# Kernel optimization log

Hardware: AMD Instinct MI355X
Metric: run time of the kernel (lower is better)

The kernel has to match this reference:

```python
import jax, jax.numpy as jnp
import numpy as np

N, K, D = 131072, 1024, 128
COMMITMENT_COST = 0.25


def setup_inputs() -> dict:
    key = jax.random.key(0)
    k1, k2 = jax.random.split(key)
    c_input = jax.random.normal(k1, (N, D), dtype=jnp.float32)
    # nn.Embedding weight initialized N(0, 0.1)
    embedding_weight = jax.random.normal(k2, (K, D), dtype=jnp.float32) * 0.1
    return {"c_input": c_input, "embedding_weight": embedding_weight}


def reference(c_input, embedding_weight):
    distances = (
        jnp.sum(c_input ** 2, axis=1, keepdims=True)
        + jnp.sum(embedding_weight ** 2, axis=1)
        - 2.0 * jnp.matmul(c_input, embedding_weight.T)
    )
    encoding_indices = jnp.argmin(distances, axis=1)  # [N]
    encodings = jax.nn.one_hot(encoding_indices, K, dtype=c_input.dtype)  # [N, K]
    # one-hot @ weight == direct gather
    quantized = embedding_weight[encoding_indices]  # [N, D]
    e_latent_loss = jnp.mean((jax.lax.stop_gradient(quantized) - c_input) ** 2)
    q_latent_loss = jnp.mean((quantized - jax.lax.stop_gradient(c_input)) ** 2)
    loss = q_latent_loss + COMMITMENT_COST * e_latent_loss
    # straight-through estimator
    quantized_st = c_input + jax.lax.stop_gradient(quantized - c_input)
    return (loss, quantized_st, encodings)
```

## Files before the change

kernel.cpp:

```cpp
#include <hip/hip_runtime.h>
#include <hip/hip_bf16.h>

#define NROWS 131072
#define KC 1024
#define DD 128
#define MARGIN 1e-3f

typedef __attribute__((ext_vector_type(8))) short short8;
typedef __attribute__((ext_vector_type(4))) float f32x4;

__device__ inline short f2bf_hi(float f) {
  unsigned u = __builtin_bit_cast(unsigned, f);
  u += 0x7fffu + ((u >> 16) & 1u);
  return (short)(u >> 16);
}
__device__ inline float bf2f(short s) {
  unsigned u = ((unsigned)(unsigned short)s) << 16;
  return __builtin_bit_cast(float, u);
}

__global__ void vq_prep(const float* __restrict__ E, short* __restrict__ EH,
                        short* __restrict__ EL, float* __restrict__ SE,
                        float* __restrict__ out) {
  int b = blockIdx.x, t = threadIdx.x;
  if (b < 64) {
    int idx = b * 256 + t;
    int s = (idx >> 6) & 3, l = idx & 63;
    int c = idx >> 8;
    int q = l >> 4, n = l & 15;
    const float* src = E + (16 * c + n) * DD + 32 * s + 8 * q;
    short8 h, lo;
#pragma unroll
    for (int j = 0; j < 8; ++j) {
      float x = src[j];
      short hb = f2bf_hi(x);
      h[j] = hb;
      lo[j] = f2bf_hi(x - bf2f(hb));
    }
    *(short8*)(EH + idx * 8) = h;
    *(short8*)(EL + idx * 8) = lo;
  } else {
    if (t == 0) out[0] = 0.f;
    for (int k = t; k < KC; k += 256) {
      double acc = 0.0;
      const float* er = E + k * DD;
      for (int i = 0; i < DD; ++i) { double v = (double)er[i]; acc += v * v; }
      SE[k] = (float)acc;
    }
  }
}

__global__ __launch_bounds__(256, 4) void vq_main(
    const float* __restrict__ X, const float* __restrict__ E,
    const short* __restrict__ EH, const short* __restrict__ EL,
    const float* __restrict__ SE, float* __restrict__ out) {
  __shared__ __align__(16) short lbh[8192];
  __shared__ __align__(16) short lbl[8192];
  __shared__ __align__(16) float lse[KC];
  __shared__ int lidx[128];
  __shared__ int lflag[128];
  __shared__ int lany;
  __shared__ float lx[128];
  __shared__ float lrv[4];
  __shared__ int lri[4];
  __shared__ float lsx;
  __shared__ float lloss[4];

  const int tid = threadIdx.x;
  const int w = tid >> 6, l = tid & 63, q = l >> 4, n = l & 15;
  const int row_base = blockIdx.x * 128;
  const int rot = blockIdx.x & 15;
  const int encb = 1 + NROWS * DD;
  if (tid == 0) lany = 0;
  *(f32x4*)(lse + tid * 4) = *(const f32x4*)(SE + tid * 4);

  float* zb = out + encb + row_base * KC;
  if (tid < 3) __builtin_nontemporal_store(0.f, zb + tid);
  else if (tid == 3) __builtin_nontemporal_store(0.f, zb + 131071);
  float* zb4 = zb + 3;

  short8 ah[2][4], al[2][4];
#pragma unroll
  for (int mt = 0; mt < 2; ++mt) {
    const float* xp = X + (row_base + 32 * w + 16 * mt + n) * DD + 8 * q;
#pragma unroll
    for (int s = 0; s < 4; ++s) {
      f32x4 x0 = *(const f32x4*)(xp + 32 * s);
      f32x4 x1 = *(const f32x4*)(xp + 32 * s + 4);
#pragma unroll
      for (int j = 0; j < 4; ++j) {
        short hb = f2bf_hi(x0[j]);
        ah[mt][s][j] = hb;
        al[mt][s][j] = f2bf_hi(x0[j] - bf2f(hb));
        short hb2 = f2bf_hi(x1[j]);
        ah[mt][s][j + 4] = hb2;
        al[mt][s][j + 4] = f2bf_hi(x1[j] - bf2f(hb2));
      }
    }
  }

  float bestv[8], secv[8];
  int besti[8];
#pragma unroll
  for (int i = 0; i < 8; ++i) { bestv[i] = -3e38f; secv[i] = -3e38f; besti[i] = 0; }

  const f32x4 z4 = {0.f, 0.f, 0.f, 0.f};
  for (int cc = 0; cc < 16; ++cc) {
    const int ccr = (cc + rot) & 15;
    {
      const short8* gh = (const short8*)(EH + ccr * 8192);
      const short8* gl = (const short8*)(EL + ccr * 8192);
      short8* dh = (short8*)lbh;
      short8* dl = (short8*)lbl;
#pragma unroll
      for (int i = 0; i < 4; ++i) {
        int u = i * 256 + tid;
        dh[u] = gh[u];
        dl[u] = gl[u];
      }
    }
    __syncthreads();

    {
      int jb = cc * 2048 + tid;
#pragma unroll
      for (int u2 = 0; u2 < 8; ++u2) {
        int j = jb + u2 * 256;
        if (j < 32767) __builtin_nontemporal_store(z4, (f32x4*)(zb4 + 4 * j));
      }
    }

#pragma unroll
    for (int nt = 0; nt < 4; ++nt) {
      f32x4 a0 = {0.f, 0.f, 0.f, 0.f}, a1 = {0.f, 0.f, 0.f, 0.f};
#pragma unroll
      for (int s = 0; s < 4; ++s) {
        short8 bh  = *(const short8*)(lbh + ((nt * 4 + s) * 64 + l) * 8);
        short8 blo = *(const short8*)(lbl + ((nt * 4 + s) * 64 + l) * 8);
        a0 = __builtin_amdgcn_mfma_f32_16x16x32_bf16(ah[0][s], bh,  a0, 0, 0, 0);
        a1 = __builtin_amdgcn_mfma_f32_16x16x32_bf16(ah[1][s], bh,  a1, 0, 0, 0);
        a0 = __builtin_amdgcn_mfma_f32_16x16x32_bf16(al[0][s], bh,  a0, 0, 0, 0);
        a1 = __builtin_amdgcn_mfma_f32_16x16x32_bf16(al[1][s], bh,  a1, 0, 0, 0);
        a0 = __builtin_amdgcn_mfma_f32_16x16x32_bf16(ah[0][s], blo, a0, 0, 0, 0);
        a1 = __builtin_amdgcn_mfma_f32_16x16x32_bf16(ah[1][s], blo, a1, 0, 0, 0);
      }
      int k = ccr * 64 + nt * 16 + n;
      float hse = 0.5f * lse[k];
#pragma unroll
      for (int r = 0; r < 4; ++r) {
        {
          float sc = a0[r] - hse;
          bool gt = sc > bestv[r];
          secv[r] = gt ? bestv[r] : fmaxf(secv[r], sc);
          if (gt) { bestv[r] = sc; besti[r] = k; }
        }
        {
          int sl = 4 + r;
          float sc = a1[r] - hse;
          bool gt = sc > bestv[sl];
          secv[sl] = gt ? bestv[sl] : fmaxf(secv[sl], sc);
          if (gt) { bestv[sl] = sc; besti[sl] = k; }
        }
      }
    }
    __syncthreads();
  }

#pragma unroll
  for (int slot = 0; slot < 8; ++slot) {
    float v = bestv[slot], s2 = secv[slot];
    int bi = besti[slot];
#pragma unroll
    for (int m = 1; m <= 8; m <<= 1) {
      float v2 = __shfl_xor(v, m, 64);
      float sv2 = __shfl_xor(s2, m, 64);
      int i2 = __shfl_xor(bi, m, 64);
      float ns = fmaxf(fminf(v, v2), fmaxf(s2, sv2));
      if (v2 > v || (v2 == v && i2 < bi)) { v = v2; bi = i2; }
      s2 = ns;
    }
    if (n == 0) {
      int mt = slot >> 2, r = slot & 3;
      int rl = 32 * w + 16 * mt + 4 * q + r;
      int f = (v - s2) <= MARGIN;
      lidx[rl] = bi;
      lflag[rl] = f;
      if (f) lany = 1;
    }
  }
  __syncthreads();

  if (lany) {
    for (int rl = 0; rl < 128; ++rl) {
      if (lflag[rl] == 0) continue;
      if (tid < DD) lx[tid] = X[(row_base + rl) * DD + tid];
      __syncthreads();
      if (tid < 64) {
        double v0 = lx[tid], v1 = lx[tid + 64];
        double s = v0 * v0 + v1 * v1;
#pragma unroll
        for (int m = 1; m < 64; m <<= 1) s += __shfl_xor(s, m, 64);
        if (tid == 0) lsx = (float)s;
      }
      __syncthreads();
      float dmin = 3e38f; int kmin = 0;
      for (int kk = tid; kk < KC; kk += 256) {
        double dot = 0.0;
        const float* er = E + kk * DD;
        for (int i = 0; i < DD; ++i) dot += (double)lx[i] * (double)er[i];
        float a = lsx + lse[kk];
        float b2 = (float)(2.0 * dot);
        float dnp = a - b2;
        if (dnp < dmin) { dmin = dnp; kmin = kk; }
      }
#pragma unroll
      for (int m = 1; m < 64; m <<= 1) {
        float v2 = __shfl_xor(dmin, m, 64);
        int k2 = __shfl_xor(kmin, m, 64);
        if (v2 < dmin || (v2 == dmin && k2 < kmin)) { dmin = v2; kmin = k2; }
      }
      if (l == 0) { lrv[w] = dmin; lri[w] = kmin; }
      __syncthreads();
      if (tid == 0) {
        float dm = lrv[0]; int km = lri[0];
#pragma unroll
        for (int t2 = 1; t2 < 4; ++t2)
          if (lrv[t2] < dm || (lrv[t2] == dm && lri[t2] < km)) { dm = lrv[t2]; km = lri[t2]; }
        lidx[rl] = km;
      }
      __syncthreads();
    }
  }
  __syncthreads();

  float lp = 0.f;
  for (int rl = w; rl < 128; rl += 4) {
    int row = row_base + rl;
    int idx = lidx[rl];
    float x0 = X[row * DD + l];
    float x1 = X[row * DD + 64 + l];
    float e0 = E[idx * DD + l];
    float e1 = E[idx * DD + 64 + l];
    float d0 = e0 - x0, d1 = e1 - x1;
    __builtin_nontemporal_store(x0 + d0, out + 1 + row * DD + l);
    __builtin_nontemporal_store(x1 + d1, out + 1 + row * DD + 64 + l);
    lp += d0 * d0 + d1 * d1;
    if (l == (idx & 63)) out[encb + row * KC + idx] = 1.f;
  }
#pragma unroll
  for (int m = 1; m < 64; m <<= 1) lp += __shfl_xor(lp, m, 64);
  if (l == 0) lloss[w] = lp;
  __syncthreads();
  if (tid == 0) {
    float t = (lloss[0] + lloss[1] + lloss[2] + lloss[3]) *
              (1.25f / ((float)NROWS * (float)DD));
    atomicAdd(out, t);
  }
}

extern "C" void kernel_launch(void* const* d_in, const int* in_sizes, int n_in,
                              void* d_out, int out_size, void* d_ws, size_t ws_size,
                              hipStream_t stream) {
  const float* X = (const float*)d_in[0];
  const float* E = (const float*)d_in[1];
  float* out = (float*)d_out;
  short* EH = (short*)d_ws;
  short* EL = EH + KC * DD;
  float* SE = (float*)(EL + KC * DD);
  vq_prep<<<65, 256, 0, stream>>>(E, EH, EL, SE, out);
  vq_main<<<NROWS / 128, 256, 0, stream>>>(X, E, EH, EL, SE, out);
}
```

Baseline: 786.7 us.

## Read codebook fragments directly from global memory, dropping LDS staging and barriers

Result: slower. 928.3 us (+18.0%).

```diff
diff --git a/kernel.cpp b/kernel.cpp
--- a/kernel.cpp
+++ b/kernel.cpp
@@ -54,9 +54,6 @@
     const float* __restrict__ X, const float* __restrict__ E,
     const short* __restrict__ EH, const short* __restrict__ EL,
     const float* __restrict__ SE, float* __restrict__ out) {
-  __shared__ __align__(16) short lbh[8192];
-  __shared__ __align__(16) short lbl[8192];
-  __shared__ __align__(16) float lse[KC];
   __shared__ int lidx[128];
   __shared__ int lflag[128];
   __shared__ int lany;
@@ -72,7 +69,6 @@
   const int rot = blockIdx.x & 15;
   const int encb = 1 + NROWS * DD;
   if (tid == 0) lany = 0;
-  *(f32x4*)(lse + tid * 4) = *(const f32x4*)(SE + tid * 4);
 
   float* zb = out + encb + row_base * KC;
   if (tid < 3) __builtin_nontemporal_store(0.f, zb + tid);
@@ -107,36 +103,20 @@
   const f32x4 z4 = {0.f, 0.f, 0.f, 0.f};
   for (int cc = 0; cc < 16; ++cc) {
     const int ccr = (cc + rot) & 15;
-    {
-      const short8* gh = (const short8*)(EH + ccr * 8192);
-      const short8* gl = (const short8*)(EL + ccr * 8192);
-      short8* dh = (short8*)lbh;
-      short8* dl = (short8*)lbl;
-#pragma unroll
-      for (int i = 0; i < 4; ++i) {
-        int u = i * 256 + tid;
-        dh[u] = gh[u];
-        dl[u] = gl[u];
-      }
-    }
-    __syncthreads();
-
-    {
-      int jb = cc * 2048 + tid;
-#pragma unroll
-      for (int u2 = 0; u2 < 8; ++u2) {
-        int j = jb + u2 * 256;
-        if (j < 32767) __builtin_nontemporal_store(z4, (f32x4*)(zb4 + 4 * j));
-      }
-    }
+    const short* bhb = EH + ccr * 8192;
+    const short* blb = EL + ccr * 8192;
+
+    float hse[4];
+#pragma unroll
+    for (int nt = 0; nt < 4; ++nt) hse[nt] = 0.5f * SE[ccr * 64 + nt * 16 + n];
 
 #pragma unroll
     for (int nt = 0; nt < 4; ++nt) {
       f32x4 a0 = {0.f, 0.f, 0.f, 0.f}, a1 = {0.f, 0.f, 0.f, 0.f};
 #pragma unroll
       for (int s = 0; s < 4; ++s) {
-        short8 bh  = *(const short8*)(lbh + ((nt * 4 + s) * 64 + l) * 8);
-        short8 blo = *(const short8*)(lbl + ((nt * 4 + s) * 64 + l) * 8);
+        short8 bh  = *(const short8*)(bhb + ((nt * 4 + s) * 64 + l) * 8);
+        short8 blo = *(const short8*)(blb + ((nt * 4 + s) * 64 + l) * 8);
         a0 = __builtin_amdgcn_mfma_f32_16x16x32_bf16(ah[0][s], bh,  a0, 0, 0, 0);
         a1 = __builtin_amdgcn_mfma_f32_16x16x32_bf16(ah[1][s], bh,  a1, 0, 0, 0);
         a0 = __builtin_amdgcn_mfma_f32_16x16x32_bf16(al[0][s], bh,  a0, 0, 0, 0);
@@ -145,26 +125,30 @@
         a1 = __builtin_amdgcn_mfma_f32_16x16x32_bf16(ah[1][s], blo, a1, 0, 0, 0);
       }
       int k = ccr * 64 + nt * 16 + n;
-      float hse = 0.5f * lse[k];
 #pragma unroll
       for (int r = 0; r < 4; ++r) {
         {
-          float sc = a0[r] - hse;
+          float sc = a0[r] - hse[nt];
           bool gt = sc > bestv[r];
           secv[r] = gt ? bestv[r] : fmaxf(secv[r], sc);
           if (gt) { bestv[r] = sc; besti[r] = k; }
         }
         {
           int sl = 4 + r;
-          float sc = a1[r] - hse;
+          float sc = a1[r] - hse[nt];
           bool gt = sc > bestv[sl];
           secv[sl] = gt ? bestv[sl] : fmaxf(secv[sl], sc);
           if (gt) { bestv[sl] = sc; besti[sl] = k; }
         }
       }
-    }
-    __syncthreads();
-  }
+#pragma unroll
+      for (int h = 0; h < 2; ++h) {
+        int j = cc * 2048 + (nt * 2 + h) * 256 + tid;
+        if (j < 32767) __builtin_nontemporal_store(z4, (f32x4*)(zb4 + 4 * j));
+      }
+    }
+  }
+  __syncthreads();
 
 #pragma unroll
   for (int slot = 0; slot < 8; ++slot) {
@@ -208,7 +192,7 @@
         double dot = 0.0;
         const float* er = E + kk * DD;
         for (int i = 0; i < DD; ++i) dot += (double)lx[i] * (double)er[i];
-        float a = lsx + lse[kk];
+        float a = lsx + SE[kk];
         float b2 = (float)(2.0 * dot);
         float dnp = a - b2;
         if (dnp < dmin) { dmin = dnp; kmin = kk; }
```
